# Performance work log

Measured on AMD Instinct MI355X. Metric: run time of the kernel, lower is better.

## Reference

```python
import jax, jax.numpy as jnp
import numpy as np

N = 4096          # nodes (= Mamba sequence length)
E_EDGES = 65536   # edges
D = 512           # dim_h (= d_inner, expand=1)
NEXP = 4          # num_experts (cfg.model.num_experts)
DSTATE = 16
DCONV = 4
DTRANK = 32       # ceil(D/16)
EPS = 1e-5


def _silu(x):
    return x * jax.nn.sigmoid(x)


def _bn(h, g, b):
    # BatchNorm1d over node axis (batch statistics)
    mu = h.mean(0)
    var = h.var(0)
    return (h - mu) * jax.lax.rsqrt(var + EPS) * g + b


def _mamba(u, in_w, conv_w, conv_b, x_w, dt_w, dt_b, A_log, Dp, out_w):
    # u: [L, D] single-sequence Mamba(d_model=D, d_state=16, d_conv=4, expand=1)
    L = u.shape[0]
    xz = u @ in_w                      # [L, 2D]
    xc, z = xz[:, :D], xz[:, D:]
    xp = jnp.pad(xc, ((DCONV - 1, 0), (0, 0)))
    xconv = conv_b
    for k in range(DCONV):             # depthwise causal conv, tiny fixed loop
        xconv = xconv + conv_w[:, k] * xp[k:k + L]
    xs = _silu(xconv)                  # [L, D]
    dbc = xs @ x_w                     # [L, DTRANK + 2*DSTATE]
    dt = jax.nn.softplus(dbc[:, :DTRANK] @ dt_w + dt_b)          # [L, D]
    Bm = dbc[:, DTRANK:DTRANK + DSTATE]                          # [L, S]
    Cm = dbc[:, DTRANK + DSTATE:]                                # [L, S]
    A = -jnp.exp(A_log)                                          # [D, S]
    dA = jnp.exp(dt[:, :, None] * A[None])                       # [L, D, S]
    dBu = dt[:, :, None] * Bm[:, None, :] * xs[:, :, None]       # [L, D, S]

    def step(hprev, inp):
        dA_t, dBu_t, C_t = inp
        hn = dA_t * hprev + dBu_t
        return hn, (hn * C_t[None, :]).sum(-1)

    _, ys = jax.lax.scan(step, jnp.zeros((D, DSTATE), u.dtype), (dA, dBu, Cm))
    y = ys + Dp * xs
    return (y * _silu(z)) @ out_w      # [L, D]


def setup_inputs() -> dict:
    key = jax.random.key(0)
    ks = jax.random.split(key, 24)
    s = 1.0 / np.sqrt(D)
    inp = {}
    inp['x'] = jax.random.normal(ks[0], (N, D), jnp.float32)
    inp['edge_index'] = jax.random.randint(ks[1], (2, E_EDGES), 0, N)
    inp['edge_attr'] = jax.random.normal(ks[2], (E_EDGES, D), jnp.float32)
    # GINE nn: Linear(D,D) -> ReLU -> Linear(D,D)
    inp['gin_w1'] = jax.random.normal(ks[3], (D, D)) * s
    inp['gin_b1'] = jnp.zeros((D,))
    inp['gin_w2'] = jax.random.normal(ks[4], (D, D)) * s
    inp['gin_b2'] = jnp.zeros((D,))
    # BatchNorms
    inp['bn1l_g'] = jnp.ones((D,)); inp['bn1l_b'] = jnp.zeros((D,))
    inp['bn1a_g'] = jnp.ones((D,)); inp['bn1a_b'] = jnp.zeros((D,))
    inp['bn2_g'] = jnp.ones((D,)); inp['bn2_b'] = jnp.zeros((D,))
    # gating MLP [D, D//2, NEXP]
    inp['gate_w1'] = jax.random.normal(ks[5], (D, D // 2)) * s
    inp['gate_b1'] = jnp.zeros((D // 2,))
    inp['gate_w2'] = jax.random.normal(ks[6], (D // 2, NEXP)) * (1.0 / np.sqrt(D // 2))
    inp['gate_b2'] = jnp.zeros((NEXP,))
    # stacked per-expert Mamba params
    inp['in_w'] = jax.random.normal(ks[7], (NEXP, D, 2 * D)) * s
    inp['conv_w'] = jax.random.normal(ks[8], (NEXP, D, DCONV)) * 0.5
    inp['conv_b'] = jnp.zeros((NEXP, D))
    inp['x_w'] = jax.random.normal(ks[9], (NEXP, D, DTRANK + 2 * DSTATE)) * s
    inp['dt_w'] = jax.random.normal(ks[10], (NEXP, DTRANK, D)) * (1.0 / np.sqrt(DTRANK))
    inp['dt_b'] = jax.random.normal(ks[11], (NEXP, D)) * 0.1 - 4.0
    A0 = jnp.log(jnp.arange(1, DSTATE + 1, dtype=jnp.float32))
    inp['A_log'] = jnp.broadcast_to(A0, (NEXP, D, DSTATE)).copy()
    inp['Dp'] = jnp.ones((NEXP, D))
    inp['out_w'] = jax.random.normal(ks[12], (NEXP, D, D)) * s
    # FFN
    inp['ff_w1'] = jax.random.normal(ks[13], (D, 2 * D)) * s
    inp['ff_b1'] = jnp.zeros((2 * D,))
    inp['ff_w2'] = jax.random.normal(ks[14], (2 * D, D)) * (1.0 / np.sqrt(2 * D))
    inp['ff_b2'] = jnp.zeros((D,))
    return inp


def reference(x, edge_index, edge_attr,
              gin_w1, gin_b1, gin_w2, gin_b2,
              bn1l_g, bn1l_b, bn1a_g, bn1a_b, bn2_g, bn2_b,
              gate_w1, gate_b1, gate_w2, gate_b2,
              in_w, conv_w, conv_b, x_w, dt_w, dt_b, A_log, Dp, out_w,
              ff_w1, ff_b1, ff_w2, ff_b2):
    h_in = x
    src, dst = edge_index[0], edge_index[1]
    # local GINEConv: nn(x + sum_j relu(x_j + e_ji))
    msg = jax.nn.relu(x[src] + edge_attr)                      # [E, D]
    aggr = jax.ops.segment_sum(msg, dst, num_segments=N)       # [N, D]
    h_local = jax.nn.relu((x + aggr) @ gin_w1 + gin_b1) @ gin_w2 + gin_b2
    h_local = _bn(h_in + h_local, bn1l_g, bn1l_b)
    # gated mixture of Mamba experts
    gate = jax.nn.softmax(jax.nn.relu(x @ gate_w1 + gate_b1) @ gate_w2 + gate_b2, axis=-1)  # [N, NEXP]
    ys = jax.vmap(_mamba, in_axes=(None, 0, 0, 0, 0, 0, 0, 0, 0, 0))(
        x, in_w, conv_w, conv_b, x_w, dt_w, dt_b, A_log, Dp, out_w)  # [NEXP, N, D]
    h_attn = jnp.einsum('ne,end->nd', gate, ys)
    h_attn = _bn(h_in + h_attn, bn1a_g, bn1a_b)
    # fuse + FFN
    h = h_local + h_attn
    ff = jax.nn.relu(h @ ff_w1 + ff_b1) @ ff_w2 + ff_b2
    return _bn(h + ff, bn2_g, bn2_b)
```

## Files before the change

kernel.cpp:

```cpp
#include <hip/hip_runtime.h>
#include <hip/hip_bf16.h>
#include <math.h>

#define N_NODES 4096
#define E_EDGE 65536
#define D 512
#define NEXP 4
#define DSTATE 16
#define DCONV 4
#define DTRANK 32
#define EPS 1e-5f
#define LCHUNK 32
#define NCHUNK (N_NODES / LCHUNK)

typedef __hip_bfloat16 bf16;
typedef short bf16x8 __attribute__((ext_vector_type(8)));
typedef float f32x4 __attribute__((ext_vector_type(4)));
typedef unsigned short u16x4 __attribute__((ext_vector_type(4)));

__device__ __forceinline__ float siluf(float x) { return x / (1.f + __expf(-x)); }
__device__ __forceinline__ float softplusf(float x) {
  return (x > 20.f) ? x : log1pf(__expf(x));
}
__device__ __forceinline__ unsigned short f2bf(float v) {
  bf16 b = __float2bfloat16(v);
  return *reinterpret_cast<unsigned short*>(&b);
}

__device__ __forceinline__ void gload16(const void* g, void* l) {
  __builtin_amdgcn_global_load_lds(
      (const __attribute__((address_space(1))) void*)g,
      (__attribute__((address_space(3))) void*)l, 16, 0, 0);
}

template <int FN, int EPI, bool STATS>
__global__ __launch_bounds__(256, 2) void mm_k(
    const bf16* __restrict__ A, int lda, long sA,
    const bf16* __restrict__ Bt, int ldb, long sB,
    const float* __restrict__ bias,
    float* __restrict__ Cf, bf16* __restrict__ Cb, int ldc, long sC, int K,
    const float* __restrict__ part, float* __restrict__ sacc) {
  constexpr int BN = FN * 32;
  __shared__ __align__(16) bf16 As[2][128 * 32];
  __shared__ __align__(16) bf16 Bs[2][BN * 32];
  const int z = blockIdx.z;
  A += (size_t)z * sA;
  Bt += (size_t)z * sB;
  const int tid = threadIdx.x;
  const int w = tid >> 6, l = tid & 63;
  const int wr = w >> 1, wc = w & 1;
  const int bm = blockIdx.y * 128, bn = blockIdx.x * BN;

  f32x4 acc[4][FN];
#pragma unroll
  for (int i = 0; i < 4; ++i)
#pragma unroll
    for (int j = 0; j < FN; ++j) acc[i][j] = 0.f;

  const int srow = l >> 2, schunk = l & 3;
  const bf16* gA = A + (size_t)(bm + w * 16 + srow) * lda + schunk * 8;
  const bf16* gB = Bt + (size_t)(bn + w * 16 + srow) * ldb + schunk * 8;

  const int ar = wr * 64 + (l & 15);
  const int br = wc * FN * 16 + (l & 15);
  const int kb = l >> 4;

  auto stage = [&](int b, int k0) {
    gload16(gA + k0, As[b] + w * 512);
    gload16(gA + k0 + (size_t)64 * lda, As[b] + 64 * 32 + w * 512);
    gload16(gB + k0, Bs[b] + w * 512);
    if (FN == 4) gload16(gB + k0 + (size_t)64 * ldb, Bs[b] + 64 * 32 + w * 512);
  };

  stage(0, 0);
  __syncthreads();
  int cur = 0;
  for (int k0 = 0; k0 < K; k0 += 32) {
    if (k0 + 32 < K) stage(cur ^ 1, k0 + 32);
    const bf16x8* Ap = (const bf16x8*)As[cur];
    const bf16x8* Bp = (const bf16x8*)Bs[cur];
    bf16x8 af[4], bfr[FN];
#pragma unroll
    for (int i = 0; i < 4; ++i) af[i] = Ap[(ar + i * 16) * 4 + kb];
#pragma unroll
    for (int j = 0; j < FN; ++j) bfr[j] = Bp[(br + j * 16) * 4 + kb];
#pragma unroll
    for (int i = 0; i < 4; ++i)
#pragma unroll
      for (int j = 0; j < FN; ++j)
        acc[i][j] = __builtin_amdgcn_mfma_f32_16x16x32_bf16(bfr[j], af[i], acc[i][j], 0, 0, 0);
    __syncthreads();
    cur ^= 1;
  }

  if (Cf) Cf += (size_t)z * sC;
  if (Cb) Cb += (size_t)z * sC;
  const int r0 = bm + wr * 64 + (l & 15);
  const int cb0 = bn + wc * FN * 16 + ((l >> 4) << 2);
  f32x4 ssum[FN], ssq[FN];
  if (STATS) {
#pragma unroll
    for (int j = 0; j < FN; ++j) { ssum[j] = 0.f; ssq[j] = 0.f; }
  }
#pragma unroll
  for (int i = 0; i < 4; ++i) {
    const int row = r0 + i * 16;
#pragma unroll
    for (int j = 0; j < FN; ++j) {
      const int col = cb0 + j * 16;
      f32x4 v = acc[i][j];
      if (bias) v += *(const f32x4*)&bias[col];
      if (EPI == 1) {
#pragma unroll
        for (int r = 0; r < 4; ++r) v[r] = fmaxf(v[r], 0.f);
      }
      if (Cf) *(f32x4*)&Cf[(size_t)row * ldc + col] = v;
      if (Cb) {
        u16x4 u;
#pragma unroll
        for (int r = 0; r < 4; ++r) u[r] = f2bf(v[r]);
        *(u16x4*)&Cb[(size_t)row * ldc + col] = u;
      }
      if (STATS) {
        f32x4 p = *(const f32x4*)&part[(size_t)row * ldc + col];
        f32x4 t = v + p;
        ssum[j] += t;
        ssq[j] += t * t;
      }
    }
  }
  if (STATS) {
#pragma unroll
    for (int m = 1; m < 16; m <<= 1) {
#pragma unroll
      for (int j = 0; j < FN; ++j)
#pragma unroll
        for (int r = 0; r < 4; ++r) {
          ssum[j][r] += __shfl_xor(ssum[j][r], m);
          ssq[j][r] += __shfl_xor(ssq[j][r], m);
        }
    }
    if ((l & 15) == 0) {
#pragma unroll
      for (int j = 0; j < FN; ++j)
#pragma unroll
        for (int r = 0; r < 4; ++r) {
          atomicAdd(&sacc[cb0 + j * 16 + r], ssum[j][r]);
          atomicAdd(&sacc[512 + cb0 + j * 16 + r], ssq[j][r]);
        }
    }
  }
}

struct WtArgs {
  const float* in[8];
  bf16* out[8];
  int K[8], N[8], ldo[8];
  long sin[8], sout[8];
  int cum[8];
};
__global__ __launch_bounds__(256) void wtrans_all_k(WtArgs a) {
  __shared__ float t[32][33];
  int b = blockIdx.x;
  int i = 0;
  while (b >= a.cum[i]) ++i;
  int local = b - (i ? a.cum[i - 1] : 0);
  const int ntx = a.N[i] / 32;
  const int nty = a.K[i] / 32;
  const int perz = ntx * nty;
  const int z = local / perz;
  const int rem = local - z * perz;
  const int bx = rem % ntx, by = rem / ntx;
  const float* in = a.in[i] + (size_t)z * a.sin[i];
  bf16* out = a.out[i] + (size_t)z * a.sout[i];
  const int N = a.N[i], ldo = a.ldo[i];
  const int n0 = bx * 32, k0 = by * 32;
  const int tx = threadIdx.x & 31, ty = threadIdx.x >> 5;
  for (int r = ty; r < 32; r += 8) t[r][tx] = in[(size_t)(k0 + r) * N + n0 + tx];
  __syncthreads();
  for (int r = ty; r < 32; r += 8)
    out[(size_t)(n0 + r) * ldo + k0 + tx] = __float2bfloat16(t[tx][r]);
}

__global__ void hist_k(const int* __restrict__ ei, int* __restrict__ deg) {
  int e = blockIdx.x * 256 + threadIdx.x;
  if (e < E_EDGE) atomicAdd(&deg[ei[E_EDGE + e]], 1);
}

__global__ __launch_bounds__(1024) void prefix_k(const int* __restrict__ deg,
                                                 int* __restrict__ rowstart) {
  __shared__ int s[1024];
  int t = threadIdx.x;
  int base = t * 4;
  int d0 = deg[base], d1 = deg[base + 1], d2 = deg[base + 2], d3 = deg[base + 3];
  int sum = d0 + d1 + d2 + d3;
  s[t] = sum;
  __syncthreads();
  for (int off = 1; off < 1024; off <<= 1) {
    int v = (t >= off) ? s[t - off] : 0;
    __syncthreads();
    s[t] += v;
    __syncthreads();
  }
  int excl = s[t] - sum;
  rowstart[base] = excl;
  rowstart[base + 1] = excl + d0;
  rowstart[base + 2] = excl + d0 + d1;
  rowstart[base + 3] = excl + d0 + d1 + d2;
}

__global__ void scatter_k(const int* __restrict__ ei, const int* __restrict__ rowstart,
                          int* __restrict__ cnt, int* __restrict__ eid) {
  int e = blockIdx.x * 256 + threadIdx.x;
  if (e < E_EDGE) {
    int dst = ei[E_EDGE + e];
    int slot = rowstart[dst] + atomicAdd(&cnt[dst], 1);
    eid[slot] = e;
  }
}

__global__ __launch_bounds__(256) void aggr_gather_k(
    const float* __restrict__ x, const int* __restrict__ ei, const float* __restrict__ ea,
    const int* __restrict__ rowstart, const int* __restrict__ deg,
    const int* __restrict__ eid, bf16* __restrict__ hpre, bf16* __restrict__ xbf) {
  int n = blockIdx.x;
  int tid = threadIdx.x;
  int beg = rowstart[n];
  int end = beg + deg[n];
  float a0 = 0.f, a1 = 0.f;
  int i = beg;
  for (; i + 1 < end; i += 2) {
    int e0 = eid[i], e1 = eid[i + 1];
    int s0 = ei[e0], s1 = ei[e1];
    const float* x0 = x + (size_t)s0 * D;
    const float* e0p = ea + (size_t)e0 * D;
    const float* x1 = x + (size_t)s1 * D;
    const float* e1p = ea + (size_t)e1 * D;
    a0 += fmaxf(x0[tid] + e0p[tid], 0.f) + fmaxf(x1[tid] + e1p[tid], 0.f);
    a1 += fmaxf(x0[tid + 256] + e0p[tid + 256], 0.f) +
          fmaxf(x1[tid + 256] + e1p[tid + 256], 0.f);
  }
  if (i < end) {
    int e0 = eid[i];
    int s0 = ei[e0];
    const float* x0 = x + (size_t)s0 * D;
    const float* e0p = ea + (size_t)e0 * D;
    a0 += fmaxf(x0[tid] + e0p[tid], 0.f);
    a1 += fmaxf(x0[tid + 256] + e0p[tid + 256], 0.f);
  }
  float xv0 = x[(size_t)n * D + tid];
  float xv1 = x[(size_t)n * D + tid + 256];
  hpre[(size_t)n * D + tid] = __float2bfloat16(xv0 + a0);
  hpre[(size_t)n * D + tid + 256] = __float2bfloat16(xv1 + a1);
  xbf[(size_t)n * D + tid] = __float2bfloat16(xv0);
  xbf[(size_t)n * D + tid + 256] = __float2bfloat16(xv1);
}

__global__ __launch_bounds__(256) void gate2_k(const float* __restrict__ g1,
                                               const float* __restrict__ w2,
                                               const float* __restrict__ b2,
                                               float* __restrict__ gate) {
  int row = blockIdx.x * 4 + (threadIdx.x >> 6);
  int lane = threadIdx.x & 63;
  float a0 = 0.f, a1 = 0.f, a2 = 0.f, a3 = 0.f;
  for (int k = lane; k < 256; k += 64) {
    float v = g1[(size_t)row * 256 + k];
    a0 = fmaf(v, w2[k * 4 + 0], a0);
    a1 = fmaf(v, w2[k * 4 + 1], a1);
    a2 = fmaf(v, w2[k * 4 + 2], a2);
    a3 = fmaf(v, w2[k * 4 + 3], a3);
  }
#pragma unroll
  for (int off = 32; off; off >>= 1) {
    a0 += __shfl_down(a0, off);
    a1 += __shfl_down(a1, off);
    a2 += __shfl_down(a2, off);
    a3 += __shfl_down(a3, off);
  }
  if (lane == 0) {
    float l0 = a0 + b2[0], l1 = a1 + b2[1], l2 = a2 + b2[2], l3 = a3 + b2[3];
    float m = fmaxf(fmaxf(l0, l1), fmaxf(l2, l3));
    float e0 = __expf(l0 - m), e1 = __expf(l1 - m), e2 = __expf(l2 - m), e3 = __expf(l3 - m);
    float s = 1.f / (e0 + e1 + e2 + e3);
    gate[row * 4 + 0] = e0 * s;
    gate[row * 4 + 1] = e1 * s;
    gate[row * 4 + 2] = e2 * s;
    gate[row * 4 + 3] = e3 * s;
  }
}

__global__ void conv_silu_k(const bf16* __restrict__ xz, const float* __restrict__ cw,
                            const float* __restrict__ cb, bf16* __restrict__ xs, int e0) {
  const int z = blockIdx.y;
  xz += (size_t)z * N_NODES * 2 * D;
  xs += (size_t)z * N_NODES * D;
  cw += (size_t)(e0 + z) * D * DCONV;
  cb += (size_t)(e0 + z) * D;
  int idx = blockIdx.x * blockDim.x + threadIdx.x;
  if (idx >= N_NODES * D) return;
  int t = idx >> 9;
  int d = idx & (D - 1);
  float acc = cb[d];
#pragma unroll
  for (int k = 0; k < DCONV; ++k) {
    int tt = t + k - (DCONV - 1);
    if (tt >= 0)
      acc = fmaf(cw[d * DCONV + k], __bfloat162float(xz[(size_t)tt * (2 * D) + d]), acc);
  }
  xs[idx] = __float2bfloat16(siluf(acc));
}

__global__ void dt_k(const float* __restrict__ dbc, const float* __restrict__ dtw,
                     const float* __restrict__ dtbias, bf16* __restrict__ dt, int e0) {
  const int z = blockIdx.y;
  dbc += (size_t)z * N_NODES * 64;
  dt += (size_t)z * N_NODES * D;
  dtw += (size_t)(e0 + z) * DTRANK * D;
  dtbias += (size_t)(e0 + z) * D;
  int idx = blockIdx.x * blockDim.x + threadIdx.x;
  int t = idx >> 9, d = idx & (D - 1);
  float acc = dtbias[d];
#pragma unroll
  for (int k = 0; k < DTRANK; ++k) acc = fmaf(dbc[t * 64 + k], dtw[k * D + d], acc);
  dt[idx] = __float2bfloat16(softplusf(acc));
}

__device__ __forceinline__ void bn_params(const float* acc, int d, float& mu, float& rsig) {
  mu = acc[d] * (1.f / N_NODES);
  float var = acc[512 + d] * (1.f / N_NODES) - mu * mu;
  rsig = rsqrtf(var + EPS);
}

__global__ void norm_k(const float* __restrict__ p, const float* __restrict__ q,
                       const float* __restrict__ acc, const float* __restrict__ g,
                       const float* __restrict__ b, float* __restrict__ o) {
  int idx = blockIdx.x * blockDim.x + threadIdx.x;
  if (idx >= N_NODES * D) return;
  int d = idx & (D - 1);
  float mu, rsig;
  bn_params(acc, d, mu, rsig);
  o[idx] = (p[idx] + q[idx] - mu) * rsig * g[d] + b[d];
}

__global__ void bnadd2_k(const float* __restrict__ x, const float* __restrict__ hloc,
                         const float* __restrict__ hattn, const float* __restrict__ acc1,
                         const float* __restrict__ acc2, const float* __restrict__ g1,
                         const float* __restrict__ b1, const float* __restrict__ g2,
                         const float* __restrict__ b2, float* __restrict__ of,
                         bf16* __restrict__ ob) {
  int idx = blockIdx.x * blockDim.x + threadIdx.x;
  if (idx >= N_NODES * D) return;
  int d = idx & (D - 1);
  float mu1, rs1, mu2, rs2;
  bn_params(acc1, d, mu1, rs1);
  bn_params(acc2, d, mu2, rs2);
  float xv = x[idx];
  float v = (xv + hloc[idx] - mu1) * rs1 * g1[d] + b1[d] +
            (xv + hattn[idx] - mu2) * rs2 * g2[d] + b2[d];
  of[idx] = v;
  ob[idx] = __float2bfloat16(v);
}

__global__ __launch_bounds__(512) void scanA_k(const bf16* __restrict__ dt,
                                               const bf16* __restrict__ xs,
                                               const float* __restrict__ dbc,
                                               const float* __restrict__ Alog,
                                               float* __restrict__ Q,
                                               float* __restrict__ dtsum, int e0) {
  const int z = blockIdx.y;
  dt += (size_t)z * N_NODES * D;
  xs += (size_t)z * N_NODES * D;
  dbc += (size_t)z * N_NODES * 64;
  Alog += (size_t)(e0 + z) * D * DSTATE;
  Q += (size_t)z * NCHUNK * D * DSTATE;
  dtsum += (size_t)z * NCHUNK * D;
  int c = blockIdx.x;
  int d = threadIdx.x;
  float As[DSTATE], h[DSTATE];
#pragma unroll
  for (int s = 0; s < DSTATE; ++s) {
    As[s] = -__expf(Alog[d * DSTATE + s]);
    h[s] = 0.f;
  }
  float dts = 0.f;
  int t0 = c * LCHUNK;
  for (int t = t0; t < t0 + LCHUNK; ++t) {
    float dtv = __bfloat162float(dt[(size_t)t * D + d]);
    float xv = __bfloat162float(xs[(size_t)t * D + d]);
    float bx = dtv * xv;
    dts += dtv;
#pragma unroll
    for (int s = 0; s < DSTATE; ++s) {
      float Bv = dbc[(size_t)t * 64 + DTRANK + s];
      h[s] = fmaf(__expf(dtv * As[s]), h[s], bx * Bv);
    }
  }
  size_t base = ((size_t)c * D + d) * DSTATE;
#pragma unroll
  for (int s = 0; s < DSTATE; ++s) Q[base + s] = h[s];
  dtsum[c * D + d] = dts;
}

__global__ __launch_bounds__(256) void scanB_k(const float* __restrict__ Q,
                                               const float* __restrict__ dtsum,
                                               const float* __restrict__ Alog,
                                               float* __restrict__ Hin, int e0) {
  const int z = blockIdx.y;
  Q += (size_t)z * NCHUNK * D * DSTATE;
  dtsum += (size_t)z * NCHUNK * D;
  Alog += (size_t)(e0 + z) * D * DSTATE;
  Hin += (size_t)z * NCHUNK * D * DSTATE;
  int idx = blockIdx.x * blockDim.x + threadIdx.x;
  int d = idx >> 4;
  float As = -__expf(Alog[idx]);
  float h = 0.f;
  for (int c = 0; c < NCHUNK; ++c) {
    size_t base = (size_t)c * D * DSTATE + idx;
    Hin[base] = h;
    h = fmaf(__expf(As * dtsum[c * D + d]), h, Q[base]);
  }
}

__global__ __launch_bounds__(512) void scanC_k(const bf16* __restrict__ dt,
                                               const bf16* __restrict__ xs,
                                               const float* __restrict__ dbc,
                                               const float* __restrict__ Alog,
                                               const float* __restrict__ Hin,
                                               const bf16* __restrict__ xz,
                                               const float* __restrict__ Dp,
                                               const float* __restrict__ gate,
                                               bf16* __restrict__ u, int e0) {
  const int z = blockIdx.y;
  dt += (size_t)z * N_NODES * D;
  xs += (size_t)z * N_NODES * D;
  dbc += (size_t)z * N_NODES * 64;
  Alog += (size_t)(e0 + z) * D * DSTATE;
  Hin += (size_t)z * NCHUNK * D * DSTATE;
  xz += (size_t)z * N_NODES * 2 * D;
  Dp += (size_t)(e0 + z) * D;
  u += (size_t)(e0 + z) * 512;
  const int ge = e0 + z;
  int c = blockIdx.x;
  int d = threadIdx.x;
  float As[DSTATE], h[DSTATE];
  size_t base = ((size_t)c * D + d) * DSTATE;
#pragma unroll
  for (int s = 0; s < DSTATE; ++s) {
    As[s] = -__expf(Alog[d * DSTATE + s]);
    h[s] = Hin[base + s];
  }
  float Dv = Dp[d];
  int t0 = c * LCHUNK;
  for (int t = t0; t < t0 + LCHUNK; ++t) {
    float dtv = __bfloat162float(dt[(size_t)t * D + d]);
    float xv = __bfloat162float(xs[(size_t)t * D + d]);
    float bx = dtv * xv;
    float y = 0.f;
#pragma unroll
    for (int s = 0; s < DSTATE; ++s) {
      float Bv = dbc[(size_t)t * 64 + DTRANK + s];
      float Cv = dbc[(size_t)t * 64 + DTRANK + DSTATE + s];
      h[s] = fmaf(__expf(dtv * As[s]), h[s], bx * Bv);
      y = fmaf(h[s], Cv, y);
    }
    float zv = __bfloat162float(xz[(size_t)t * (2 * D) + D + d]);
    float gv = gate[t * NEXP + ge];
    u[(size_t)t * 2048 + d] = __float2bfloat16(gv * (y + Dv * xv) * siluf(zv));
  }
}

extern "C" void kernel_launch(void* const* d_in, const int* in_sizes, int n_in,
                              void* d_out, int out_size, void* d_ws, size_t ws_size,
                              hipStream_t stream) {
  const float* x = (const float*)d_in[0];
  const int* ei = (const int*)d_in[1];
  const float* ea = (const float*)d_in[2];
  const float* gin_w1 = (const float*)d_in[3];
  const float* gin_b1 = (const float*)d_in[4];
  const float* gin_w2 = (const float*)d_in[5];
  const float* gin_b2 = (const float*)d_in[6];
  const float* bn1l_g = (const float*)d_in[7];
  const float* bn1l_b = (const float*)d_in[8];
  const float* bn1a_g = (const float*)d_in[9];
  const float* bn1a_b = (const float*)d_in[10];
  const float* bn2_g = (const float*)d_in[11];
  const float* bn2_b = (const float*)d_in[12];
  const float* gate_w1 = (const float*)d_in[13];
  const float* gate_b1 = (const float*)d_in[14];
  const float* gate_w2 = (const float*)d_in[15];
  const float* gate_b2 = (const float*)d_in[16];
  const float* in_w = (const float*)d_in[17];
  const float* conv_w = (const float*)d_in[18];
  const float* conv_b = (const float*)d_in[19];
  const float* x_w = (const float*)d_in[20];
  const float* dt_w = (const float*)d_in[21];
  const float* dt_b = (const float*)d_in[22];
  const float* A_log = (const float*)d_in[23];
  const float* Dp = (const float*)d_in[24];
  const float* out_w = (const float*)d_in[25];
  const float* ff_w1 = (const float*)d_in[26];
  const float* ff_b1 = (const float*)d_in[27];
  const float* ff_w2 = (const float*)d_in[28];
  const float* ff_b2 = (const float*)d_in[29];
  float* out = (float*)d_out;

  const size_t ND = (size_t)N_NODES * D;
  const size_t NDb = ND / 2;

  const size_t fixed_f = 3 * ND + (size_t)N_NODES * 256 + 16384 + 2490624 + ND + 2048 +
                         81920 + 2 * ND + 4096;
  const size_t per_f = 2 * ND + NDb + (size_t)N_NODES * 64 + NDb +
                       2 * (size_t)NCHUNK * D * DSTATE + (size_t)NCHUNK * D;
  const int EB = (ws_size >= (fixed_f + 4 * per_f + 65536) * sizeof(float)) ? 4 : 1;

  float* ws = (float*)d_ws;
  size_t off = 0;
  auto alloc = [&](size_t n) {
    float* p = ws + off;
    off += (n + 63) & ~(size_t)63;
    return p;
  };
  float* ffo = alloc(ND);
  float* pbuf = alloc(ND);
  float* hlocal = alloc(ND);
  float* g1 = alloc((size_t)N_NODES * 256);
  float* gate = alloc((size_t)N_NODES * NEXP);
  bf16* gw1t = (bf16*)alloc(131072);
  bf16* gw2t = (bf16*)alloc(131072);
  bf16* gatew1t = (bf16*)alloc(65536);
  bf16* inwt = (bf16*)alloc(1048576);
  bf16* xwt = (bf16*)alloc(65536);
  bf16* outwt_cat = (bf16*)alloc(524288);
  bf16* ffw1t = (bf16*)alloc(262144);
  bf16* ffw2t = (bf16*)alloc(262144);
  int* deg = (int*)alloc(N_NODES);
  int* cnt = (int*)alloc(N_NODES);
  float* accs = alloc(3072);
  int* eid = (int*)alloc(E_EDGE);
  int* rowstart = (int*)alloc(N_NODES);
  float* xbf_f = alloc(NDb);
  float* xz_f = alloc((size_t)EB * ND);
  float* xs_f = alloc((size_t)EB * NDb);
  float* dbc = alloc((size_t)EB * N_NODES * 64);
  float* dtb_f = alloc((size_t)EB * NDb);
  float* Qb = alloc((size_t)EB * NCHUNK * D * DSTATE);
  float* Hin = alloc((size_t)EB * NCHUNK * D * DSTATE);
  float* dtsum = alloc((size_t)EB * NCHUNK * D);
  float* ucat_f = alloc(4 * NDb);
  float* hattn_raw = alloc(ND);
  float* acc1 = accs, *acc2 = accs + 1024, *acc3 = accs + 2048;

  bf16* x_bf = (bf16*)xbf_f;
  bf16* hpre_bf = (bf16*)pbuf;
  bf16* t1_bf = (bf16*)(pbuf + NDb);
  bf16* xz_bf = (bf16*)xz_f;
  bf16* xs_bf = (bf16*)xs_f;
  bf16* dt_bf = (bf16*)dtb_f;
  bf16* ucat = (bf16*)ucat_f;
  float* hcomb = xz_f;
  bf16* hcomb_bf = (bf16*)(ucat_f);
  bf16* ffh_bf = (bf16*)pbuf;

  const int nelem = N_NODES * D;
  const int ew = (nelem + 255) / 256;

  hipMemsetAsync(deg, 0, (N_NODES + N_NODES + 3072) * sizeof(float), stream);

  WtArgs wa;
  const float* wsrc[8] = {gin_w1, gin_w2, gate_w1, in_w, x_w, out_w, ff_w1, ff_w2};
  bf16* wdst[8] = {gw1t, gw2t, gatew1t, inwt, xwt, outwt_cat, ffw1t, ffw2t};
  int wK[8] = {512, 512, 512, 512, 512, 512, 512, 1024};
  int wN[8] = {512, 512, 256, 1024, 64, 512, 1024, 512};
  int wldo[8] = {512, 512, 512, 512, 512, 2048, 512, 1024};
  long wsin[8] = {0, 0, 0, (long)512 * 1024, (long)512 * 64, (long)512 * 512, 0, 0};
  long wsout[8] = {0, 0, 0, (long)512 * 1024, (long)64 * 512, 512, 0, 0};
  int wz[8] = {1, 1, 1, 4, 4, 4, 1, 1};
  int cum = 0;
  for (int i = 0; i < 8; ++i) {
    wa.in[i] = wsrc[i];
    wa.out[i] = wdst[i];
    wa.K[i] = wK[i];
    wa.N[i] = wN[i];
    wa.ldo[i] = wldo[i];
    wa.sin[i] = wsin[i];
    wa.sout[i] = wsout[i];
    cum += (wN[i] / 32) * (wK[i] / 32) * wz[i];
    wa.cum[i] = cum;
  }
  wtrans_all_k<<<cum, 256, 0, stream>>>(wa);

  hist_k<<<E_EDGE / 256, 256, 0, stream>>>(ei, deg);
  prefix_k<<<1, 1024, 0, stream>>>(deg, rowstart);
  scatter_k<<<E_EDGE / 256, 256, 0, stream>>>(ei, rowstart, cnt, eid);
  aggr_gather_k<<<N_NODES, 256, 0, stream>>>(x, ei, ea, rowstart, deg, eid, hpre_bf, x_bf);
  mm_k<2, 1, false><<<dim3(8, 32, 1), 256, 0, stream>>>(
      hpre_bf, 512, 0, gw1t, 512, 0, gin_b1, nullptr, t1_bf, 512, 0, 512, nullptr,
      nullptr);
  mm_k<2, 0, true><<<dim3(8, 32, 1), 256, 0, stream>>>(
      t1_bf, 512, 0, gw2t, 512, 0, gin_b2, hlocal, nullptr, 512, 0, 512, x, acc1);

  mm_k<2, 1, false><<<dim3(4, 32, 1), 256, 0, stream>>>(
      x_bf, 512, 0, gatew1t, 512, 0, gate_b1, g1, nullptr, 256, 0, 512, nullptr, nullptr);
  gate2_k<<<N_NODES / 4, 256, 0, stream>>>(g1, gate_w2, gate_b2, gate);

  for (int e0 = 0; e0 < NEXP; e0 += EB) {
    mm_k<4, 0, false><<<dim3(8, 32, EB), 256, 0, stream>>>(
        x_bf, 512, 0, inwt + (size_t)e0 * 512 * 1024, 512, (long)512 * 1024, nullptr,
        nullptr, xz_bf, 1024, (long)N_NODES * 1024, 512, nullptr, nullptr);
    conv_silu_k<<<dim3(ew, EB), 256, 0, stream>>>(xz_bf, conv_w, conv_b, xs_bf, e0);
    mm_k<2, 0, false><<<dim3(1, 32, EB), 256, 0, stream>>>(
        xs_bf, 512, (long)ND, xwt + (size_t)e0 * 64 * 512, 512, (long)64 * 512, nullptr,
        dbc, nullptr, 64, (long)N_NODES * 64, 512, nullptr, nullptr);
    dt_k<<<dim3(ew, EB), 256, 0, stream>>>(dbc, dt_w, dt_b, dt_bf, e0);
    scanA_k<<<dim3(NCHUNK, EB), 512, 0, stream>>>(dt_bf, xs_bf, dbc, A_log, Qb, dtsum, e0);
    scanB_k<<<dim3((D * DSTATE) / 256, EB), 256, 0, stream>>>(Qb, dtsum, A_log, Hin, e0);
    scanC_k<<<dim3(NCHUNK, EB), 512, 0, stream>>>(dt_bf, xs_bf, dbc, A_log, Hin, xz_bf, Dp,
                                                  gate, ucat, e0);
  }
  mm_k<2, 0, true><<<dim3(8, 32, 1), 256, 0, stream>>>(
      ucat, 2048, 0, outwt_cat, 2048, 0, nullptr, hattn_raw, nullptr, 512, 0, 2048, x,
      acc2);

  bnadd2_k<<<ew, 256, 0, stream>>>(x, hlocal, hattn_raw, acc1, acc2, bn1l_g, bn1l_b,
                                   bn1a_g, bn1a_b, hcomb, hcomb_bf);
  mm_k<4, 1, false><<<dim3(8, 32, 1), 256, 0, stream>>>(
      hcomb_bf, 512, 0, ffw1t, 512, 0, ff_b1, nullptr, ffh_bf, 1024, 0, 512, nullptr,
      nullptr);
  mm_k<2, 0, true><<<dim3(8, 32, 1), 256, 0, stream>>>(
      ffh_bf, 1024, 0, ffw2t, 1024, 0, ff_b2, ffo, nullptr, 512, 0, 1024, hcomb, acc3);
  norm_k<<<ew, 256, 0, stream>>>(hcomb, ffo, acc3, bn2_g, bn2_b, out);
}
```

Measured before the change: 464.6 us.

## Group independent GEMMs into multi-problem launches and vectorize conv/dt kernels

```diff
diff --git a/kernel.cpp b/kernel.cpp
--- a/kernel.cpp
+++ b/kernel.cpp
@@ -25,6 +25,11 @@
 __device__ __forceinline__ unsigned short f2bf(float v) {
   bf16 b = __float2bfloat16(v);
   return *reinterpret_cast<unsigned short*>(&b);
+}
+__device__ __forceinline__ float bfu2f(unsigned short u) {
+  bf16 b;
+  *reinterpret_cast<unsigned short*>(&b) = u;
+  return __bfloat162float(b);
 }
 
 __device__ __forceinline__ void gload16(const void* g, void* l) {
@@ -147,6 +152,137 @@
         for (int r = 0; r < 4; ++r) {
           atomicAdd(&sacc[cb0 + j * 16 + r], ssum[j][r]);
           atomicAdd(&sacc[512 + cb0 + j * 16 + r], ssq[j][r]);
+        }
+    }
+  }
+}
+
+struct MmArgs {
+  const bf16* A[4];
+  const bf16* Bt[4];
+  const float* bias[4];
+  float* Cf[4];
+  bf16* Cb[4];
+  const float* part[4];
+  float* sacc[4];
+  long sA[4], sB[4], sC[4];
+  int lda[4], ldb[4], ldc[4], K[4], epi[4], stats[4], gx[4], cum[4];
+};
+__global__ __launch_bounds__(256, 2) void mgemm_k(MmArgs a) {
+  __shared__ __align__(16) bf16 As[2][128 * 32];
+  __shared__ __align__(16) bf16 Bs[2][64 * 32];
+  int b = blockIdx.x;
+  int i = 0;
+  while (b >= a.cum[i]) ++i;
+  int local = b - (i ? a.cum[i - 1] : 0);
+  const int perz = a.gx[i] * 32;
+  const int z = local / perz;
+  const int rem = local - z * perz;
+  const int by = rem / a.gx[i];
+  const int bx = rem - by * a.gx[i];
+  const int lda = a.lda[i], ldb = a.ldb[i], ldc = a.ldc[i], K = a.K[i];
+  const bf16* A = a.A[i] + (size_t)z * a.sA[i];
+  const bf16* Bt = a.Bt[i] + (size_t)z * a.sB[i];
+
+  const int tid = threadIdx.x;
+  const int w = tid >> 6, l = tid & 63;
+  const int wr = w >> 1, wc = w & 1;
+  const int bm = by * 128, bn = bx * 64;
+
+  f32x4 acc[4][2];
+#pragma unroll
+  for (int p = 0; p < 4; ++p)
+#pragma unroll
+    for (int j = 0; j < 2; ++j) acc[p][j] = 0.f;
+
+  const int srow = l >> 2, schunk = l & 3;
+  const bf16* gA = A + (size_t)(bm + w * 16 + srow) * lda + schunk * 8;
+  const bf16* gB = Bt + (size_t)(bn + w * 16 + srow) * ldb + schunk * 8;
+
+  const int ar = wr * 64 + (l & 15);
+  const int br = wc * 32 + (l & 15);
+  const int kb = l >> 4;
+
+  auto stage = [&](int bb, int k0) {
+    gload16(gA + k0, As[bb] + w * 512);
+    gload16(gA + k0 + (size_t)64 * lda, As[bb] + 64 * 32 + w * 512);
+    gload16(gB + k0, Bs[bb] + w * 512);
+  };
+
+  stage(0, 0);
+  __syncthreads();
+  int cur = 0;
+  for (int k0 = 0; k0 < K; k0 += 32) {
+    if (k0 + 32 < K) stage(cur ^ 1, k0 + 32);
+    const bf16x8* Ap = (const bf16x8*)As[cur];
+    const bf16x8* Bp = (const bf16x8*)Bs[cur];
+    bf16x8 af[4], bfr[2];
+#pragma unroll
+    for (int p = 0; p < 4; ++p) af[p] = Ap[(ar + p * 16) * 4 + kb];
+#pragma unroll
+    for (int j = 0; j < 2; ++j) bfr[j] = Bp[(br + j * 16) * 4 + kb];
+#pragma unroll
+    for (int p = 0; p < 4; ++p)
+#pragma unroll
+      for (int j = 0; j < 2; ++j)
+        acc[p][j] = __builtin_amdgcn_mfma_f32_16x16x32_bf16(bfr[j], af[p], acc[p][j], 0, 0, 0);
+    __syncthreads();
+    cur ^= 1;
+  }
+
+  float* Cf = a.Cf[i] ? a.Cf[i] + (size_t)z * a.sC[i] : nullptr;
+  bf16* Cb = a.Cb[i] ? a.Cb[i] + (size_t)z * a.sC[i] : nullptr;
+  const float* bias = a.bias[i];
+  const int epi = a.epi[i], stats = a.stats[i];
+  const int r0 = bm + wr * 64 + (l & 15);
+  const int cb0 = bn + wc * 32 + ((l >> 4) << 2);
+  f32x4 ssum[2], ssq[2];
+  ssum[0] = 0.f; ssum[1] = 0.f; ssq[0] = 0.f; ssq[1] = 0.f;
+#pragma unroll
+  for (int p = 0; p < 4; ++p) {
+    const int row = r0 + p * 16;
+#pragma unroll
+    for (int j = 0; j < 2; ++j) {
+      const int col = cb0 + j * 16;
+      f32x4 v = acc[p][j];
+      if (bias) v += *(const f32x4*)&bias[col];
+      if (epi == 1) {
+#pragma unroll
+        for (int r = 0; r < 4; ++r) v[r] = fmaxf(v[r], 0.f);
+      }
+      if (Cf) *(f32x4*)&Cf[(size_t)row * ldc + col] = v;
+      if (Cb) {
+        u16x4 u;
+#pragma unroll
+        for (int r = 0; r < 4; ++r) u[r] = f2bf(v[r]);
+        *(u16x4*)&Cb[(size_t)row * ldc + col] = u;
+      }
+      if (stats) {
+        f32x4 pp = *(const f32x4*)&a.part[i][(size_t)row * ldc + col];
+        f32x4 t = v + pp;
+        ssum[j] += t;
+        ssq[j] += t * t;
+      }
+    }
+  }
+  if (stats) {
+#pragma unroll
+    for (int m = 1; m < 16; m <<= 1) {
+#pragma unroll
+      for (int j = 0; j < 2; ++j)
+#pragma unroll
+        for (int r = 0; r < 4; ++r) {
+          ssum[j][r] += __shfl_xor(ssum[j][r], m);
+          ssq[j][r] += __shfl_xor(ssq[j][r], m);
+        }
+    }
+    if ((l & 15) == 0) {
+#pragma unroll
+      for (int j = 0; j < 2; ++j)
+#pragma unroll
+        for (int r = 0; r < 4; ++r) {
+          atomicAdd(&a.sacc[i][cb0 + j * 16 + r], ssum[j][r]);
+          atomicAdd(&a.sacc[i][512 + cb0 + j * 16 + r], ssq[j][r]);
         }
     }
   }
@@ -297,17 +433,25 @@
   cw += (size_t)(e0 + z) * D * DCONV;
   cb += (size_t)(e0 + z) * D;
   int idx = blockIdx.x * blockDim.x + threadIdx.x;
-  if (idx >= N_NODES * D) return;
-  int t = idx >> 9;
-  int d = idx & (D - 1);
-  float acc = cb[d];
+  if (idx >= N_NODES * (D / 4)) return;
+  int t = idx >> 7;
+  int d4 = (idx & 127) << 2;
+  float a[4];
+#pragma unroll
+  for (int j = 0; j < 4; ++j) a[j] = cb[d4 + j];
 #pragma unroll
   for (int k = 0; k < DCONV; ++k) {
     int tt = t + k - (DCONV - 1);
-    if (tt >= 0)
-      acc = fmaf(cw[d * DCONV + k], __bfloat162float(xz[(size_t)tt * (2 * D) + d]), acc);
-  }
-  xs[idx] = __float2bfloat16(siluf(acc));
+    if (tt >= 0) {
+      u16x4 v = *(const u16x4*)&xz[(size_t)tt * (2 * D) + d4];
+#pragma unroll
+      for (int j = 0; j < 4; ++j) a[j] = fmaf(cw[(d4 + j) * DCONV + k], bfu2f(v[j]), a[j]);
+    }
+  }
+  u16x4 o;
+#pragma unroll
+  for (int j = 0; j < 4; ++j) o[j] = f2bf(siluf(a[j]));
+  *(u16x4*)&xs[(size_t)t * D + d4] = o;
 }
 
 __global__ void dt_k(const float* __restrict__ dbc, const float* __restrict__ dtw,
@@ -318,11 +462,20 @@
   dtw += (size_t)(e0 + z) * DTRANK * D;
   dtbias += (size_t)(e0 + z) * D;
   int idx = blockIdx.x * blockDim.x + threadIdx.x;
-  int t = idx >> 9, d = idx & (D - 1);
-  float acc = dtbias[d];
-#pragma unroll
-  for (int k = 0; k < DTRANK; ++k) acc = fmaf(dbc[t * 64 + k], dtw[k * D + d], acc);
-  dt[idx] = __float2bfloat16(softplusf(acc));
+  if (idx >= N_NODES * (D / 4)) return;
+  int t = idx >> 7;
+  int d4 = (idx & 127) << 2;
+  f32x4 a = *(const f32x4*)&dtbias[d4];
+#pragma unroll
+  for (int k = 0; k < DTRANK; ++k) {
+    float b = dbc[t * 64 + k];
+    f32x4 wv = *(const f32x4*)&dtw[k * D + d4];
+    a += b * wv;
+  }
+  u16x4 o;
+#pragma unroll
+  for (int j = 0; j < 4; ++j) o[j] = f2bf(softplusf(a[j]));
+  *(u16x4*)&dt[(size_t)t * D + d4] = o;
 }
 
 __device__ __forceinline__ void bn_params(const float* acc, int d, float& mu, float& rsig) {
@@ -563,6 +716,7 @@
 
   const int nelem = N_NODES * D;
   const int ew = (nelem + 255) / 256;
+  const int ew4 = (nelem / 4 + 255) / 256;
 
   hipMemsetAsync(deg, 0, (N_NODES + N_NODES + 3072) * sizeof(float), stream);
 
@@ -593,30 +747,81 @@
   prefix_k<<<1, 1024, 0, stream>>>(deg, rowstart);
   scatter_k<<<E_EDGE / 256, 256, 0, stream>>>(ei, rowstart, cnt, eid);
   aggr_gather_k<<<N_NODES, 256, 0, stream>>>(x, ei, ea, rowstart, deg, eid, hpre_bf, x_bf);
-  mm_k<2, 1, false><<<dim3(8, 32, 1), 256, 0, stream>>>(
-      hpre_bf, 512, 0, gw1t, 512, 0, gin_b1, nullptr, t1_bf, 512, 0, 512, nullptr,
-      nullptr);
-  mm_k<2, 0, true><<<dim3(8, 32, 1), 256, 0, stream>>>(
-      t1_bf, 512, 0, gw2t, 512, 0, gin_b2, hlocal, nullptr, 512, 0, 512, x, acc1);
-
-  mm_k<2, 1, false><<<dim3(4, 32, 1), 256, 0, stream>>>(
-      x_bf, 512, 0, gatew1t, 512, 0, gate_b1, g1, nullptr, 256, 0, 512, nullptr, nullptr);
-  gate2_k<<<N_NODES / 4, 256, 0, stream>>>(g1, gate_w2, gate_b2, gate);
-
-  for (int e0 = 0; e0 < NEXP; e0 += EB) {
-    mm_k<4, 0, false><<<dim3(8, 32, EB), 256, 0, stream>>>(
-        x_bf, 512, 0, inwt + (size_t)e0 * 512 * 1024, 512, (long)512 * 1024, nullptr,
-        nullptr, xz_bf, 1024, (long)N_NODES * 1024, 512, nullptr, nullptr);
-    conv_silu_k<<<dim3(ew, EB), 256, 0, stream>>>(xz_bf, conv_w, conv_b, xs_bf, e0);
-    mm_k<2, 0, false><<<dim3(1, 32, EB), 256, 0, stream>>>(
-        xs_bf, 512, (long)ND, xwt + (size_t)e0 * 64 * 512, 512, (long)64 * 512, nullptr,
-        dbc, nullptr, 64, (long)N_NODES * 64, 512, nullptr, nullptr);
-    dt_k<<<dim3(ew, EB), 256, 0, stream>>>(dbc, dt_w, dt_b, dt_bf, e0);
-    scanA_k<<<dim3(NCHUNK, EB), 512, 0, stream>>>(dt_bf, xs_bf, dbc, A_log, Qb, dtsum, e0);
-    scanB_k<<<dim3((D * DSTATE) / 256, EB), 256, 0, stream>>>(Qb, dtsum, A_log, Hin, e0);
-    scanC_k<<<dim3(NCHUNK, EB), 512, 0, stream>>>(dt_bf, xs_bf, dbc, A_log, Hin, xz_bf, Dp,
-                                                  gate, ucat, e0);
-  }
+
+  if (EB == 4) {
+    MmArgs m1 = {};
+    m1.A[0] = hpre_bf; m1.lda[0] = 512; m1.sA[0] = 0;
+    m1.Bt[0] = gw1t; m1.ldb[0] = 512; m1.sB[0] = 0;
+    m1.bias[0] = gin_b1; m1.Cb[0] = t1_bf; m1.ldc[0] = 512; m1.sC[0] = 0;
+    m1.K[0] = 512; m1.epi[0] = 1; m1.gx[0] = 8;
+    m1.A[1] = x_bf; m1.lda[1] = 512; m1.sA[1] = 0;
+    m1.Bt[1] = gatew1t; m1.ldb[1] = 512; m1.sB[1] = 0;
+    m1.bias[1] = gate_b1; m1.Cf[1] = g1; m1.ldc[1] = 256; m1.sC[1] = 0;
+    m1.K[1] = 512; m1.epi[1] = 1; m1.gx[1] = 4;
+    m1.A[2] = x_bf; m1.lda[2] = 512; m1.sA[2] = 0;
+    m1.Bt[2] = inwt; m1.ldb[2] = 512; m1.sB[2] = (long)512 * 1024;
+    m1.Cb[2] = xz_bf; m1.ldc[2] = 1024; m1.sC[2] = (long)N_NODES * 1024;
+    m1.K[2] = 512; m1.epi[2] = 0; m1.gx[2] = 16;
+    int c1 = 8 * 32;
+    m1.cum[0] = c1;
+    c1 += 4 * 32;
+    m1.cum[1] = c1;
+    c1 += 16 * 32 * 4;
+    m1.cum[2] = c1;
+    m1.cum[3] = c1;
+    mgemm_k<<<c1, 256, 0, stream>>>(m1);
+    gate2_k<<<N_NODES / 4, 256, 0, stream>>>(g1, gate_w2, gate_b2, gate);
+    conv_silu_k<<<dim3(ew4, 4), 256, 0, stream>>>(xz_bf, conv_w, conv_b, xs_bf, 0);
+
+    MmArgs m2 = {};
+    m2.A[0] = t1_bf; m2.lda[0] = 512; m2.sA[0] = 0;
+    m2.Bt[0] = gw2t; m2.ldb[0] = 512; m2.sB[0] = 0;
+    m2.bias[0] = gin_b2; m2.Cf[0] = hlocal; m2.ldc[0] = 512; m2.sC[0] = 0;
+    m2.K[0] = 512; m2.epi[0] = 0; m2.stats[0] = 1; m2.part[0] = x; m2.sacc[0] = acc1;
+    m2.gx[0] = 8;
+    m2.A[1] = xs_bf; m2.lda[1] = 512; m2.sA[1] = (long)ND;
+    m2.Bt[1] = xwt; m2.ldb[1] = 512; m2.sB[1] = (long)64 * 512;
+    m2.Cf[1] = dbc; m2.ldc[1] = 64; m2.sC[1] = (long)N_NODES * 64;
+    m2.K[1] = 512; m2.epi[1] = 0; m2.gx[1] = 1;
+    int c2 = 8 * 32;
+    m2.cum[0] = c2;
+    c2 += 1 * 32 * 4;
+    m2.cum[1] = c2;
+    m2.cum[2] = c2;
+    m2.cum[3] = c2;
+    mgemm_k<<<c2, 256, 0, stream>>>(m2);
+
+    dt_k<<<dim3(ew4, 4), 256, 0, stream>>>(dbc, dt_w, dt_b, dt_bf, 0);
+    scanA_k<<<dim3(NCHUNK, 4), 512, 0, stream>>>(dt_bf, xs_bf, dbc, A_log, Qb, dtsum, 0);
+    scanB_k<<<dim3((D * DSTATE) / 256, 4), 256, 0, stream>>>(Qb, dtsum, A_log, Hin, 0);
+    scanC_k<<<dim3(NCHUNK, 4), 512, 0, stream>>>(dt_bf, xs_bf, dbc, A_log, Hin, xz_bf, Dp,
+                                                 gate, ucat, 0);
+  } else {
+    mm_k<2, 1, false><<<dim3(8, 32, 1), 256, 0, stream>>>(
+        hpre_bf, 512, 0, gw1t, 512, 0, gin_b1, nullptr, t1_bf, 512, 0, 512, nullptr,
+        nullptr);
+    mm_k<2, 0, true><<<dim3(8, 32, 1), 256, 0, stream>>>(
+        t1_bf, 512, 0, gw2t, 512, 0, gin_b2, hlocal, nullptr, 512, 0, 512, x, acc1);
+    mm_k<2, 1, false><<<dim3(4, 32, 1), 256, 0, stream>>>(
+        x_bf, 512, 0, gatew1t, 512, 0, gate_b1, g1, nullptr, 256, 0, 512, nullptr,
+        nullptr);
+    gate2_k<<<N_NODES / 4, 256, 0, stream>>>(g1, gate_w2, gate_b2, gate);
+    for (int e0 = 0; e0 < NEXP; ++e0) {
+      mm_k<4, 0, false><<<dim3(8, 32, 1), 256, 0, stream>>>(
+          x_bf, 512, 0, inwt + (size_t)e0 * 512 * 1024, 512, 0, nullptr, nullptr, xz_bf,
+          1024, 0, 512, nullptr, nullptr);
+      conv_silu_k<<<dim3(ew4, 1), 256, 0, stream>>>(xz_bf, conv_w, conv_b, xs_bf, e0);
+      mm_k<2, 0, false><<<dim3(1, 32, 1), 256, 0, stream>>>(
+          xs_bf, 512, 0, xwt + (size_t)e0 * 64 * 512, 512, 0, nullptr, dbc, nullptr, 64,
+          0, 512, nullptr, nullptr);
+      dt_k<<<dim3(ew4, 1), 256, 0, stream>>>(dbc, dt_w, dt_b, dt_bf, e0);
+      scanA_k<<<dim3(NCHUNK, 1), 512, 0, stream>>>(dt_bf, xs_bf, dbc, A_log, Qb, dtsum, e0);
+      scanB_k<<<dim3((D * DSTATE) / 256, 1), 256, 0, stream>>>(Qb, dtsum, A_log, Hin, e0);
+      scanC_k<<<dim3(NCHUNK, 1), 512, 0, stream>>>(dt_bf, xs_bf, dbc, A_log, Hin, xz_bf,
+                                                   Dp, gate, ucat, e0);
+    }
+  }
+
   mm_k<2, 0, true><<<dim3(8, 32, 1), 256, 0, stream>>>(
       ucat, 2048, 0, outwt_cat, 2048, 0, nullptr, hattn_raw, nullptr, 512, 0, 2048, x,
       acc2);
```

After: 457.9 us. No clear change (-1.4%).
